# Kernel tuning notes

Measured on AMD Instinct MI355X. Metric: run time of the kernel, lower is better.

The kernel has to match this reference:

```python
import jax, jax.numpy as jnp
import numpy as np

B, T, D = 4, 8192, 1024
H = 16
HD = D // H  # 64
TOP_K = 64


def setup_inputs() -> dict:
    key = jax.random.key(0)
    ks = jax.random.split(key, 6)
    x = jax.random.normal(ks[0], (B, T, D), dtype=jnp.float32)
    # torch nn.Linear weights are [out, in]; y = x @ W.T
    Wq = jax.random.normal(ks[1], (D, D), dtype=jnp.float32) * 0.02
    Wk = jax.random.normal(ks[2], (D, D), dtype=jnp.float32) * 0.02
    Wv = jax.random.normal(ks[3], (D, D), dtype=jnp.float32) * 0.02
    Wo = jax.random.normal(ks[4], (D, D), dtype=jnp.float32) * 0.02
    # indexer: nn.Linear(head_dim, 1, bias=False) -> weight [1, HD]; keep as [HD]
    w_score = jax.random.normal(ks[5], (HD,), dtype=jnp.float32) * 0.02
    return {"x": x, "Wq": Wq, "Wk": Wk, "Wv": Wv, "Wo": Wo, "w_score": w_score}


def reference(x, Wq, Wk, Wv, Wo, w_score):
    b, t, d = x.shape
    top_k = min(TOP_K, t)
    # projections: [B,T,D] -> [B,H,T,HD]
    def proj(W):
        return jnp.einsum('btd,ed->bte', x, W).reshape(b, t, H, HD).transpose(0, 2, 1, 3)
    q = proj(Wq)
    k = proj(Wk)
    v = proj(Wv)
    # lightning indexer scores: [B,H,T]
    idx_scores = jnp.einsum('bhtd,d->bht', k, w_score)
    _, top_idx = jax.lax.top_k(idx_scores, top_k)  # [B,H,K]
    idx = top_idx[..., None]  # [B,H,K,1]
    k_sparse = jnp.take_along_axis(k, idx, axis=2)  # [B,H,K,HD]
    v_sparse = jnp.take_along_axis(v, idx, axis=2)
    scale = HD ** -0.5
    scores = jnp.einsum('bhtd,bhkd->bhtk', q, k_sparse) * scale  # [B,H,T,K]
    attn = jax.nn.softmax(scores, axis=-1)
    out = jnp.einsum('bhtk,bhkd->bhtd', attn, v_sparse)  # [B,H,T,HD]
    out = out.transpose(0, 2, 1, 3).reshape(b, t, d)
    return jnp.einsum('btd,ed->bte', out, Wo)
```

## Files before the change

### kernel.cpp

```cpp
#include <hip/hip_runtime.h>
#include <hip/hip_bf16.h>
#include <stdint.h>

#define NB 4
#define NT 8192
#define ND 1024
#define NH 16
#define NHD 64
#define NK 64
#define NM (NB*NT)

typedef __attribute__((ext_vector_type(4))) float f32x4;
typedef __attribute__((ext_vector_type(8))) short s16x8;
typedef const void __attribute__((address_space(1)))* gas1_t;
typedef void __attribute__((address_space(3)))* las3_t;

__device__ __forceinline__ float bf2f(ushort u) {
  union { uint32_t i; float f; } v; v.i = ((uint32_t)u) << 16; return v.f;
}
__device__ __forceinline__ ushort f2bf(float f) {
  union { float f; uint32_t i; } v; v.f = f;
  uint32_t r = v.i + 0x7FFFu + ((v.i >> 16) & 1u);
  return (ushort)(r >> 16);
}
__device__ __forceinline__ uint32_t f2ord(uint32_t u) {
  return (u & 0x80000000u) ? ~u : (u | 0x80000000u);
}

__global__ __launch_bounds__(256) void convert_w_kernel(
    const float* __restrict__ Wq, const float* __restrict__ Wk,
    const float* __restrict__ Wv, const float* __restrict__ Wo,
    ushort* __restrict__ wqb, ushort* __restrict__ wkb,
    ushort* __restrict__ wvb, ushort* __restrict__ wob) {
  int i = blockIdx.x * 256 + threadIdx.x;
  wqb[i] = f2bf(Wq[i]); wkb[i] = f2bf(Wk[i]);
  wvb[i] = f2bf(Wv[i]); wob[i] = f2bf(Wo[i]);
}

__global__ __launch_bounds__(256) void prep_u_kernel(
    const float* __restrict__ Wk, const float* __restrict__ wscore,
    ushort* __restrict__ uhi, ushort* __restrict__ ulo) {
  int e = (blockIdx.x & 3) * 256 + threadIdx.x;
  int h = blockIdx.x >> 2;
  float acc = 0.f;
  #pragma unroll 8
  for (int d = 0; d < NHD; ++d) acc += wscore[d] * Wk[(size_t)(h*NHD + d)*ND + e];
  ushort hv = f2bf(acc);
  uhi[h*ND + e] = hv;
  ulo[h*ND + e] = f2bf(acc - bf2f(hv));
}

__global__ __launch_bounds__(256) void prep_x_kernel(
    const float* __restrict__ x, const ushort* __restrict__ uhi,
    const ushort* __restrict__ ulo, ushort* __restrict__ xb,
    float* __restrict__ scores) {
  __shared__ __align__(16) ushort Ahi[32 * 128];
  __shared__ __align__(16) ushort Alo[32 * 128];
  __shared__ float red[4][2][16][17];
  int t = threadIdx.x, w = t >> 6, l = t & 63;
  int tok0 = blockIdx.x * 32;
  int srow = t >> 3;
  int sg = (t & 7) * 2;
  int rs = l & 15, ks8 = (l >> 4) * 8;
  f32x4 acc[2];
  acc[0] = (f32x4){0.f,0.f,0.f,0.f};
  acc[1] = (f32x4){0.f,0.f,0.f,0.f};
  for (int kc = 0; kc < 8; ++kc) {
    int kb = kc * 128;
    {
      const float* xr = x + (size_t)(tok0 + srow) * ND + kb + sg * 8;
      f32x4 v0 = *(const f32x4*)xr;
      f32x4 v1 = *(const f32x4*)(xr + 4);
      f32x4 v2 = *(const f32x4*)(xr + 8);
      f32x4 v3 = *(const f32x4*)(xr + 12);
      s16x8 hi0, lo0, hi1, lo1;
      #pragma unroll
      for (int j = 0; j < 4; ++j) {
        ushort h;
        h = f2bf(v0[j]); hi0[j]   = (short)h; lo0[j]   = (short)f2bf(v0[j] - bf2f(h));
        h = f2bf(v1[j]); hi0[4+j] = (short)h; lo0[4+j] = (short)f2bf(v1[j] - bf2f(h));
        h = f2bf(v2[j]); hi1[j]   = (short)h; lo1[j]   = (short)f2bf(v2[j] - bf2f(h));
        h = f2bf(v3[j]); hi1[4+j] = (short)h; lo1[4+j] = (short)f2bf(v3[j] - bf2f(h));
      }
      ushort* xo = xb + (size_t)(tok0 + srow) * ND + kb + sg * 8;
      *(s16x8*)xo = hi0;
      *(s16x8*)(xo + 8) = hi1;
      int p0 = (sg ^ (srow & 7)) * 8, p1 = ((sg + 1) ^ (srow & 7)) * 8;
      *(s16x8*)&Ahi[srow*128 + p0] = hi0;
      *(s16x8*)&Ahi[srow*128 + p1] = hi1;
      *(s16x8*)&Alo[srow*128 + p0] = lo0;
      *(s16x8*)&Alo[srow*128 + p1] = lo1;
    }
    __syncthreads();
    {
      s16x8 bh = *(const s16x8*)(uhi + rs * ND + kb + w * 32 + ks8);
      s16x8 bl = *(const s16x8*)(ulo + rs * ND + kb + w * 32 + ks8);
      int gl = w * 4 + (l >> 4);
      #pragma unroll
      for (int mi = 0; mi < 2; ++mi) {
        int row = mi * 16 + rs;
        int gp = (gl ^ (row & 7)) * 8;
        s16x8 ah = *(const s16x8*)&Ahi[row*128 + gp];
        s16x8 al = *(const s16x8*)&Alo[row*128 + gp];
        acc[mi] = __builtin_amdgcn_mfma_f32_16x16x32_bf16(ah, bh, acc[mi], 0, 0, 0);
        acc[mi] = __builtin_amdgcn_mfma_f32_16x16x32_bf16(al, bh, acc[mi], 0, 0, 0);
        acc[mi] = __builtin_amdgcn_mfma_f32_16x16x32_bf16(ah, bl, acc[mi], 0, 0, 0);
      }
    }
    __syncthreads();
  }
  #pragma unroll
  for (int mi = 0; mi < 2; ++mi)
    #pragma unroll
    for (int r = 0; r < 4; ++r)
      red[w][mi][(l >> 4) * 4 + r][l & 15] = acc[mi][r];
  __syncthreads();
  int boff = ((tok0 >> 13) << 4);
  int tt0 = tok0 & (NT - 1);
  #pragma unroll
  for (int it = 0; it < 2; ++it) {
    int tok = t & 31, h = (t >> 5) + it * 8;
    int mi = tok >> 4, row = tok & 15;
    float s = red[0][mi][row][h] + red[1][mi][row][h]
            + red[2][mi][row][h] + red[3][mi][row][h];
    scores[(size_t)(boff + h) * NT + tt0 + tok] = s;
  }
}

__global__ __launch_bounds__(256) void topk_kernel(
    const float* __restrict__ scores, int* __restrict__ tidx) {
  int bh = blockIdx.x, t = threadIdx.x;
  __shared__ uint32_t keys[NT];
  __shared__ int hist[4096];
  __shared__ uint32_t ck[512];
  __shared__ int ci[512];
  __shared__ int chunksum[256];
  __shared__ int s_binB, s_c0;
  __shared__ int cnt_hi, cnt_cand;

  for (int i = t; i < 4096; i += 256) hist[i] = 0;
  if (t == 0) { cnt_hi = 0; cnt_cand = 0; }
  __syncthreads();
  const uint4* sg = (const uint4*)(scores + (size_t)bh * NT);
  for (int i = t; i < NT/4; i += 256) {
    uint4 v = sg[i];
    uint32_t k0 = f2ord(v.x), k1 = f2ord(v.y), k2 = f2ord(v.z), k3 = f2ord(v.w);
    keys[i*4+0] = k0; keys[i*4+1] = k1; keys[i*4+2] = k2; keys[i*4+3] = k3;
    atomicAdd(&hist[k0 >> 20], 1); atomicAdd(&hist[k1 >> 20], 1);
    atomicAdd(&hist[k2 >> 20], 1); atomicAdd(&hist[k3 >> 20], 1);
  }
  __syncthreads();
  {
    int hi = 4095 - t * 16;
    int s = 0;
    #pragma unroll
    for (int j = 0; j < 16; ++j) s += hist[hi - j];
    chunksum[t] = s;
  }
  __syncthreads();
  if (t == 0) {
    int cum = 0, c = 0;
    while (cum + chunksum[c] < NK) { cum += chunksum[c]; ++c; }
    int bin = 4095 - c * 16;
    while (cum + hist[bin] < NK) { cum += hist[bin]; --bin; }
    s_binB = bin; s_c0 = cum;
  }
  __syncthreads();
  int binB = s_binB, c0 = s_c0;
  for (int i = t; i < NT; i += 256) {
    int b = keys[i] >> 20;
    if (b > binB) {
      int p = atomicAdd(&cnt_hi, 1);
      tidx[bh*NK + p] = i;
    } else if (b == binB) {
      int p = atomicAdd(&cnt_cand, 1);
      if (p < 512) { ck[p] = keys[i]; ci[p] = i; }
    }
  }
  __syncthreads();
  int nc = cnt_cand; if (nc > 512) nc = 512;
  int need = NK - c0;
  for (int p = t; p < nc; p += 256) {
    uint32_t myk = ck[p]; int myi = ci[p];
    int rank = 0;
    for (int j = 0; j < nc; ++j) {
      uint32_t kj = ck[j];
      rank += (kj > myk || (kj == myk && ci[j] < myi)) ? 1 : 0;
    }
    if (rank < need) tidx[bh*NK + c0 + rank] = myi;
  }
}

__global__ __launch_bounds__(256, 4) void sparse_kv_kernel(
    const ushort* __restrict__ xb, const ushort* __restrict__ wkb,
    const ushort* __restrict__ wvb, const int* __restrict__ tidx,
    ushort* __restrict__ ksp, ushort* __restrict__ vtsp) {
  int bh = blockIdx.x, gy = blockIdx.y;
  int b = bh >> 4, h = bh & 15;
  int t = threadIdx.x;
  __shared__ __align__(16) ushort xl[16][128];
  __shared__ int kid[16];
  if (t < 16) kid[t] = tidx[bh*NK + gy*16 + t];
  int d = t & 63, kq = t >> 6;
  float ak[4] = {0.f,0.f,0.f,0.f}, av[4] = {0.f,0.f,0.f,0.f};
  const ushort* wkr = wkb + (size_t)(h*NHD + d) * ND;
  const ushort* wvr = wvb + (size_t)(h*NHD + d) * ND;
  for (int kc = 0; kc < ND; kc += 128) {
    __syncthreads();
    {
      int row = t >> 4, c8 = (t & 15) * 8;
      *(uint4*)&xl[row][c8] = *(const uint4*)(xb + (size_t)(b*NT + kid[row]) * ND + kc + c8);
    }
    __syncthreads();
    #pragma unroll 1
    for (int sub = 0; sub < 8; ++sub) {
      s16x8 k0 = *(const s16x8*)(wkr + kc + sub*16);
      s16x8 k1 = *(const s16x8*)(wkr + kc + sub*16 + 8);
      s16x8 v0 = *(const s16x8*)(wvr + kc + sub*16);
      s16x8 v1 = *(const s16x8*)(wvr + kc + sub*16 + 8);
      float kf[16], vf2[16];
      #pragma unroll
      for (int j = 0; j < 8; ++j) {
        kf[j]  = bf2f((ushort)k0[j]); kf[8+j]  = bf2f((ushort)k1[j]);
        vf2[j] = bf2f((ushort)v0[j]); vf2[8+j] = bf2f((ushort)v1[j]);
      }
      #pragma unroll
      for (int kk = 0; kk < 4; ++kk) {
        #pragma unroll
        for (int j = 0; j < 16; ++j) {
          float xvv = bf2f(xl[kq*4 + kk][sub*16 + j]);
          ak[kk] += xvv * kf[j];
          av[kk] += xvv * vf2[j];
        }
      }
    }
  }
  #pragma unroll
  for (int kk = 0; kk < 4; ++kk) {
    int key = gy*16 + kq*4 + kk;
    ksp[((size_t)bh*NK + key)*NHD + d] = f2bf(ak[kk]);
    vtsp[((size_t)bh*NHD + d)*NK + key] = f2bf(av[kk]);
  }
}

template<int STORE_BF16>
__global__ __launch_bounds__(512, 2) void gemm8_kernel(
    const ushort* __restrict__ A, const ushort* __restrict__ Bw,
    void* __restrict__ Cout) {
  __shared__ __align__(16) char lds[131072];
  const int t = threadIdx.x, wid = t >> 6, l = t & 63;
  const int wr = wid >> 2, wc = wid & 3;
  int bid = blockIdx.x;
  int wg = (bid & 7) * 64 + (bid >> 3);
  int tm = wg >> 2, tn = wg & 3;
  const int K = 1024, N = 1024;
  const ushort* Ab = A + (size_t)tm * 256 * K;
  const ushort* Bb = Bw + (size_t)tn * 256 * K;
  const int skh  = ((l & 3) * 8) ^ (((l >> 5) & 1) << 4);
  const int srow = l >> 2;
  const int lane_off = (l & 15) * 64 + ((((l >> 4) * 8) ^ (((l >> 3) & 1) << 4)) * 2);
  f32x4 acc[8][4];
  #pragma unroll
  for (int i = 0; i < 8; ++i)
    #pragma unroll
    for (int j = 0; j < 4; ++j) acc[i][j] = (f32x4){0.f, 0.f, 0.f, 0.f};
  s16x8 afr[4][2], bfr[2][2];

#define STG(gbase, matoff, half, ktile, buf) do { \
    const ushort* _s = (gbase) + (size_t)((half)*128 + wid*16 + srow) * K + (ktile)*64 + skh; \
    int _d = (buf)*65536 + (matoff) + ((half)*128 + wid*16)*64; \
    __builtin_amdgcn_global_load_lds((gas1_t)_s, (las3_t)(lds + _d), 16, 0, 0); \
    __builtin_amdgcn_global_load_lds((gas1_t)(_s + 32), (las3_t)(lds + _d + 16384), 16, 0, 0); \
  } while (0)

#define RD_A(mh, kh, buf) do { \
    _Pragma("unroll") \
    for (int mi = 0; mi < 4; ++mi) \
      afr[mi][kh] = *(const s16x8*)(lds + (buf)*65536 + (kh)*16384 + \
                      ((((mh)*2 + wr)*64 + mi*16))*64 + lane_off); \
  } while (0)

#define RD_B(nh, kh, buf) do { \
    _Pragma("unroll") \
    for (int ni = 0; ni < 2; ++ni) \
      bfr[ni][kh] = *(const s16x8*)(lds + (buf)*65536 + 32768 + (kh)*16384 + \
                      (((nh)*128 + wc*32 + ni*16))*64 + lane_off); \
  } while (0)

#define MMAQH(mh, nh, kh) do { \
    __builtin_amdgcn_s_setprio(1); \
    _Pragma("unroll") \
    for (int mi = 0; mi < 4; ++mi) \
      _Pragma("unroll") \
      for (int ni = 0; ni < 2; ++ni) \
        acc[(mh)*4+mi][(nh)*2+ni] = __builtin_amdgcn_mfma_f32_16x16x32_bf16( \
            afr[mi][kh], bfr[ni][kh], acc[(mh)*4+mi][(nh)*2+ni], 0, 0, 0); \
    __builtin_amdgcn_s_setprio(0); \
  } while (0)

#define LG0() do { asm volatile("s_waitcnt lgkmcnt(0)" ::: "memory"); \
                   __builtin_amdgcn_sched_barrier(0); } while (0)
#define ENDPH() do { __builtin_amdgcn_sched_barrier(0); \
                     __builtin_amdgcn_s_barrier(); } while (0)

#define TILE(kt, bc, bn) do { \
  LG0(); MMAQH(0,0,0); RD_A(0,1,bc); RD_B(0,1,bc); ENDPH(); \
  LG0(); MMAQH(0,0,1); RD_B(1,0,bc); \
  if ((kt)+1 < 16) STG(Bb,32768,0,(kt)+1,bn); ENDPH(); \
  LG0(); MMAQH(0,1,0); RD_B(1,1,bc); ENDPH(); \
  LG0(); MMAQH(0,1,1); RD_A(1,0,bc); \
  if ((kt)+2 < 16) STG(Ab,0,0,(kt)+2,bc); ENDPH(); \
  LG0(); MMAQH(1,1,0); RD_A(1,1,bc); ENDPH(); \
  LG0(); MMAQH(1,1,1); RD_B(0,0,bc); \
  if ((kt)+2 < 16) STG(Bb,32768,1,(kt)+2,bc); ENDPH(); \
  LG0(); MMAQH(1,0,0); RD_B(0,1,bc); ENDPH(); \
  LG0(); MMAQH(1,0,1); \
  if ((kt) < 14)       { asm volatile("s_waitcnt vmcnt(4)" ::: "memory"); } \
  else if ((kt) == 14) { asm volatile("s_waitcnt vmcnt(0)" ::: "memory"); } \
  __builtin_amdgcn_sched_barrier(0); \
  __builtin_amdgcn_s_barrier(); \
  if ((kt)+1 < 16) { RD_A(0,0,bn); RD_B(0,0,bn); } \
  if ((kt)+2 < 16) STG(Ab,0,1,(kt)+2,bc); \
} while (0)

  STG(Ab,0,0,0,0); STG(Bb,32768,0,0,0); STG(Ab,0,1,0,0); STG(Bb,32768,1,0,0);
  STG(Ab,0,0,1,1); STG(Bb,32768,1,1,1); STG(Ab,0,1,1,1);
  asm volatile("s_waitcnt vmcnt(6)" ::: "memory");
  __builtin_amdgcn_s_barrier();
  RD_A(0,0,0); RD_B(0,0,0);

  for (int k2 = 0; k2 < 8; ++k2) {
    TILE(2*k2,     0, 1);
    TILE(2*k2 + 1, 1, 0);
  }
#undef TILE
#undef STG
#undef RD_A
#undef RD_B
#undef MMAQH
#undef LG0
#undef ENDPH

  #pragma unroll
  for (int mi8 = 0; mi8 < 8; ++mi8) {
    int grow = tm*256 + (((mi8 >> 2)*2 + wr)*64) + (mi8 & 3)*16 + (l >> 4)*4;
    #pragma unroll
    for (int ni4 = 0; ni4 < 4; ++ni4) {
      int gcol = tn*256 + (ni4 >> 1)*128 + wc*32 + (ni4 & 1)*16 + (l & 15);
      #pragma unroll
      for (int r = 0; r < 4; ++r) {
        size_t off = (size_t)(grow + r) * N + gcol;
        if (STORE_BF16) ((ushort*)Cout)[off] = f2bf(acc[mi8][ni4][r]);
        else            ((float*)Cout)[off]  = acc[mi8][ni4][r];
      }
    }
  }
}

__global__ __launch_bounds__(256, 2) void attn_kernel(
    const ushort* __restrict__ qg, const ushort* __restrict__ ksp,
    const ushort* __restrict__ vtsp, ushort* __restrict__ aout) {
  int bh = blockIdx.y;
  int b = bh >> 4, h = bh & 15;
  int t = threadIdx.x, w = t >> 6, l = t & 63;
  __shared__ __align__(16) ushort Pl[4][1024];
  const ushort* kb = ksp + (size_t)bh * NK * NHD;
  const ushort* vb = vtsp + (size_t)bh * NHD * NK;
  s16x8 kf[2][4], vf[2][4];
  #pragma unroll
  for (int ks = 0; ks < 2; ++ks)
    #pragma unroll
    for (int ni = 0; ni < 4; ++ni) {
      kf[ks][ni] = *(const s16x8*)&kb[(size_t)(ni*16 + (l & 15))*NHD + ks*32 + (l >> 4)*8];
      vf[ks][ni] = *(const s16x8*)&vb[(size_t)(ni*16 + (l & 15))*NK + ks*32 + (l >> 4)*8];
    }
  int rowbase = blockIdx.x * 256 + w * 64;
  #pragma unroll 1
  for (int mi = 0; mi < 4; ++mi) {
    int r0 = rowbase + mi * 16;
    s16x8 af[2];
    #pragma unroll
    for (int ks = 0; ks < 2; ++ks)
      af[ks] = *(const s16x8*)&qg[(size_t)(b*NT + r0 + (l & 15))*ND + h*NHD + ks*32 + (l >> 4)*8];
    f32x4 sc[4];
    #pragma unroll
    for (int ni = 0; ni < 4; ++ni) {
      f32x4 z; z[0]=0.f; z[1]=0.f; z[2]=0.f; z[3]=0.f;
      z = __builtin_amdgcn_mfma_f32_16x16x32_bf16(af[0], kf[0][ni], z, 0, 0, 0);
      sc[ni] = __builtin_amdgcn_mfma_f32_16x16x32_bf16(af[1], kf[1][ni], z, 0, 0, 0);
    }
    #pragma unroll
    for (int r = 0; r < 4; ++r) {
      float v0 = sc[0][r]*0.125f, v1 = sc[1][r]*0.125f;
      float v2 = sc[2][r]*0.125f, v3 = sc[3][r]*0.125f;
      float m = fmaxf(fmaxf(v0, v1), fmaxf(v2, v3));
      #pragma unroll
      for (int mm = 8; mm >= 1; mm >>= 1) m = fmaxf(m, __shfl_xor(m, mm, 64));
      float e0 = __expf(v0 - m), e1 = __expf(v1 - m);
      float e2 = __expf(v2 - m), e3 = __expf(v3 - m);
      float s = e0 + e1 + e2 + e3;
      #pragma unroll
      for (int mm = 8; mm >= 1; mm >>= 1) s += __shfl_xor(s, mm, 64);
      float inv = 1.f / s;
      int prow = (l >> 4)*4 + r;
      int lo = l & 7, hb = (l >> 3) & 1, sw = prow & 7;
      Pl[w][prow*64 + ((0 + hb) ^ sw)*8 + lo] = f2bf(e0 * inv);
      Pl[w][prow*64 + ((2 + hb) ^ sw)*8 + lo] = f2bf(e1 * inv);
      Pl[w][prow*64 + ((4 + hb) ^ sw)*8 + lo] = f2bf(e2 * inv);
      Pl[w][prow*64 + ((6 + hb) ^ sw)*8 + lo] = f2bf(e3 * inv);
    }
    s16x8 pf[2];
    #pragma unroll
    for (int ks = 0; ks < 2; ++ks)
      pf[ks] = *(const s16x8*)&Pl[w][(l & 15)*64 + ((ks*4 + (l >> 4)) ^ (l & 7))*8];
    f32x4 oc[4];
    #pragma unroll
    for (int ni = 0; ni < 4; ++ni) {
      f32x4 z; z[0]=0.f; z[1]=0.f; z[2]=0.f; z[3]=0.f;
      z = __builtin_amdgcn_mfma_f32_16x16x32_bf16(pf[0], vf[0][ni], z, 0, 0, 0);
      oc[ni] = __builtin_amdgcn_mfma_f32_16x16x32_bf16(pf[1], vf[1][ni], z, 0, 0, 0);
    }
    #pragma unroll
    for (int ni = 0; ni < 4; ++ni)
      #pragma unroll
      for (int r = 0; r < 4; ++r) {
        int row = r0 + (l >> 4)*4 + r;
        aout[(size_t)(b*NT + row)*ND + h*NHD + ni*16 + (l & 15)] = f2bf(oc[ni][r]);
      }
  }
}

extern "C" void kernel_launch(void* const* d_in, const int* in_sizes, int n_in,
                              void* d_out, int out_size, void* d_ws, size_t ws_size,
                              hipStream_t stream) {
  (void)in_sizes; (void)n_in; (void)out_size; (void)ws_size;
  const float* x  = (const float*)d_in[0];
  const float* Wq = (const float*)d_in[1];
  const float* Wk = (const float*)d_in[2];
  const float* Wv = (const float*)d_in[3];
  const float* Wo = (const float*)d_in[4];
  const float* wscore = (const float*)d_in[5];

  char* base = (char*)d_ws;
  ushort* xb     = (ushort*)(base + 0);
  ushort* qb     = (ushort*)(base + 67108864);
  float*  scores = (float*) (base + 134217728);
  ushort* uhi    = (ushort*)(base + 136314880);
  ushort* ulo    = (ushort*)(base + 136347648);
  ushort* wqb    = (ushort*)(base + 136380416);
  ushort* wkb    = (ushort*)(base + 138477568);
  ushort* wvb    = (ushort*)(base + 140574720);
  ushort* wob    = (ushort*)(base + 142671872);
  int*    tidx   = (int*)   (base + 144769024);
  ushort* ksp    = (ushort*)(base + 144785408);
  ushort* vtsp   = (ushort*)(base + 145309696);
  ushort* aout   = xb;

  convert_w_kernel<<<dim3(4096), dim3(256), 0, stream>>>(Wq, Wk, Wv, Wo, wqb, wkb, wvb, wob);
  prep_u_kernel<<<dim3(64), dim3(256), 0, stream>>>(Wk, wscore, uhi, ulo);
  prep_x_kernel<<<dim3(1024), dim3(256), 0, stream>>>(x, uhi, ulo, xb, scores);
  topk_kernel<<<dim3(64), dim3(256), 0, stream>>>(scores, tidx);
  sparse_kv_kernel<<<dim3(64, 4), dim3(256), 0, stream>>>(xb, wkb, wvb, tidx, ksp, vtsp);
  gemm8_kernel<1><<<dim3(512), dim3(512), 0, stream>>>(xb, wqb, (void*)qb);
  attn_kernel<<<dim3(32, 64), dim3(256), 0, stream>>>(qb, ksp, vtsp, aout);
  gemm8_kernel<0><<<dim3(512), dim3(512), 0, stream>>>(aout, wob, d_out);
}
```

Measured before the change: 292.7 us.

## Restructure GEMM main loop into two-phase k-half schedule with fewer barriers

```diff
diff --git a/kernel.cpp b/kernel.cpp
--- a/kernel.cpp
+++ b/kernel.cpp
@@ -264,7 +264,7 @@
   for (int i = 0; i < 8; ++i)
     #pragma unroll
     for (int j = 0; j < 4; ++j) acc[i][j] = (f32x4){0.f, 0.f, 0.f, 0.f};
-  s16x8 afr[4][2], bfr[2][2];
+  s16x8 aS[2][8], bS[2][4];
 
 #define STG(gbase, matoff, half, ktile, buf) do { \
     const ushort* _s = (gbase) + (size_t)((half)*128 + wid*16 + srow) * K + (ktile)*64 + skh; \
@@ -273,73 +273,74 @@
     __builtin_amdgcn_global_load_lds((gas1_t)(_s + 32), (las3_t)(lds + _d + 16384), 16, 0, 0); \
   } while (0)
 
-#define RD_A(mh, kh, buf) do { \
+#define STGALL(ktile, buf) do { \
+    STG(Ab, 0, 0, ktile, buf);     STG(Ab, 0, 1, ktile, buf); \
+    STG(Bb, 32768, 0, ktile, buf); STG(Bb, 32768, 1, ktile, buf); \
+  } while (0)
+
+#define RD_ALLX(kh, buf) do { \
     _Pragma("unroll") \
-    for (int mi = 0; mi < 4; ++mi) \
-      afr[mi][kh] = *(const s16x8*)(lds + (buf)*65536 + (kh)*16384 + \
-                      ((((mh)*2 + wr)*64 + mi*16))*64 + lane_off); \
+    for (int mh = 0; mh < 2; ++mh) \
+      _Pragma("unroll") \
+      for (int mi = 0; mi < 4; ++mi) \
+        aS[kh][mh*4+mi] = *(const s16x8*)(lds + (buf)*65536 + (kh)*16384 + \
+                          ((mh*2 + wr)*64 + mi*16)*64 + lane_off); \
+    _Pragma("unroll") \
+    for (int nh = 0; nh < 2; ++nh) \
+      _Pragma("unroll") \
+      for (int ni = 0; ni < 2; ++ni) \
+        bS[kh][nh*2+ni] = *(const s16x8*)(lds + (buf)*65536 + 32768 + (kh)*16384 + \
+                          ((nh*128 + wc*32 + ni*16))*64 + lane_off); \
   } while (0)
 
-#define RD_B(nh, kh, buf) do { \
-    _Pragma("unroll") \
-    for (int ni = 0; ni < 2; ++ni) \
-      bfr[ni][kh] = *(const s16x8*)(lds + (buf)*65536 + 32768 + (kh)*16384 + \
-                      (((nh)*128 + wc*32 + ni*16))*64 + lane_off); \
-  } while (0)
-
-#define MMAQH(mh, nh, kh) do { \
+#define MM32(kh) do { \
     __builtin_amdgcn_s_setprio(1); \
     _Pragma("unroll") \
-    for (int mi = 0; mi < 4; ++mi) \
+    for (int mf = 0; mf < 8; ++mf) \
       _Pragma("unroll") \
-      for (int ni = 0; ni < 2; ++ni) \
-        acc[(mh)*4+mi][(nh)*2+ni] = __builtin_amdgcn_mfma_f32_16x16x32_bf16( \
-            afr[mi][kh], bfr[ni][kh], acc[(mh)*4+mi][(nh)*2+ni], 0, 0, 0); \
+      for (int nf = 0; nf < 4; ++nf) \
+        acc[mf][nf] = __builtin_amdgcn_mfma_f32_16x16x32_bf16( \
+            aS[kh][mf], bS[kh][nf], acc[mf][nf], 0, 0, 0); \
     __builtin_amdgcn_s_setprio(0); \
   } while (0)
 
-#define LG0() do { asm volatile("s_waitcnt lgkmcnt(0)" ::: "memory"); \
-                   __builtin_amdgcn_sched_barrier(0); } while (0)
-#define ENDPH() do { __builtin_amdgcn_sched_barrier(0); \
-                     __builtin_amdgcn_s_barrier(); } while (0)
-
-#define TILE(kt, bc, bn) do { \
-  LG0(); MMAQH(0,0,0); RD_A(0,1,bc); RD_B(0,1,bc); ENDPH(); \
-  LG0(); MMAQH(0,0,1); RD_B(1,0,bc); \
-  if ((kt)+1 < 16) STG(Bb,32768,0,(kt)+1,bn); ENDPH(); \
-  LG0(); MMAQH(0,1,0); RD_B(1,1,bc); ENDPH(); \
-  LG0(); MMAQH(0,1,1); RD_A(1,0,bc); \
-  if ((kt)+2 < 16) STG(Ab,0,0,(kt)+2,bc); ENDPH(); \
-  LG0(); MMAQH(1,1,0); RD_A(1,1,bc); ENDPH(); \
-  LG0(); MMAQH(1,1,1); RD_B(0,0,bc); \
-  if ((kt)+2 < 16) STG(Bb,32768,1,(kt)+2,bc); ENDPH(); \
-  LG0(); MMAQH(1,0,0); RD_B(0,1,bc); ENDPH(); \
-  LG0(); MMAQH(1,0,1); \
-  if ((kt) < 14)       { asm volatile("s_waitcnt vmcnt(4)" ::: "memory"); } \
+#define BODY(kt, bc, bn) do { \
+  RD_ALLX(1, bc);                        \
+  MM32(0);                               \
+  asm volatile("s_waitcnt lgkmcnt(0)" ::: "memory"); \
+  __builtin_amdgcn_sched_barrier(0); \
+  __builtin_amdgcn_s_barrier();          \
+  __builtin_amdgcn_sched_barrier(0); \
+  if ((kt) + 2 < 16) STGALL((kt) + 2, bc); \
+  if ((kt) < 14)       { asm volatile("s_waitcnt vmcnt(8)" ::: "memory"); } \
   else if ((kt) == 14) { asm volatile("s_waitcnt vmcnt(0)" ::: "memory"); } \
   __builtin_amdgcn_sched_barrier(0); \
-  __builtin_amdgcn_s_barrier(); \
-  if ((kt)+1 < 16) { RD_A(0,0,bn); RD_B(0,0,bn); } \
-  if ((kt)+2 < 16) STG(Ab,0,1,(kt)+2,bc); \
+  if ((kt) < 15) { \
+    __builtin_amdgcn_s_barrier();        \
+    __builtin_amdgcn_sched_barrier(0); \
+    RD_ALLX(0, bn);                      \
+  } \
+  MM32(1);                               \
+  __builtin_amdgcn_sched_barrier(0);     \
 } while (0)
 
-  STG(Ab,0,0,0,0); STG(Bb,32768,0,0,0); STG(Ab,0,1,0,0); STG(Bb,32768,1,0,0);
-  STG(Ab,0,0,1,1); STG(Bb,32768,1,1,1); STG(Ab,0,1,1,1);
-  asm volatile("s_waitcnt vmcnt(6)" ::: "memory");
+  STGALL(0, 0);
+  STGALL(1, 1);
+  asm volatile("s_waitcnt vmcnt(8)" ::: "memory");
+  __builtin_amdgcn_sched_barrier(0);
   __builtin_amdgcn_s_barrier();
-  RD_A(0,0,0); RD_B(0,0,0);
+  __builtin_amdgcn_sched_barrier(0);
+  RD_ALLX(0, 0);
 
   for (int k2 = 0; k2 < 8; ++k2) {
-    TILE(2*k2,     0, 1);
-    TILE(2*k2 + 1, 1, 0);
-  }
-#undef TILE
+    BODY(2*k2,     0, 1);
+    BODY(2*k2 + 1, 1, 0);
+  }
+#undef BODY
+#undef MM32
+#undef RD_ALLX
+#undef STGALL
 #undef STG
-#undef RD_A
-#undef RD_B
-#undef MMAQH
-#undef LG0
-#undef ENDPH
 
   #pragma unroll
   for (int mi8 = 0; mi8 < 8; ++mi8) {
```

New measurement: 399.0 us. +36.3%, slower.

## Fuse top-k selection with MFMA sparse K/V projection, merge prep_u into convert

Applied to the files above, without the earlier changes.

```diff
diff --git a/kernel.cpp b/kernel.cpp
--- a/kernel.cpp
+++ b/kernel.cpp
@@ -30,24 +30,23 @@
 __global__ __launch_bounds__(256) void convert_w_kernel(
     const float* __restrict__ Wq, const float* __restrict__ Wk,
     const float* __restrict__ Wv, const float* __restrict__ Wo,
+    const float* __restrict__ wscore,
     ushort* __restrict__ wqb, ushort* __restrict__ wkb,
-    ushort* __restrict__ wvb, ushort* __restrict__ wob) {
+    ushort* __restrict__ wvb, ushort* __restrict__ wob,
+    ushort* __restrict__ uhi, ushort* __restrict__ ulo) {
   int i = blockIdx.x * 256 + threadIdx.x;
   wqb[i] = f2bf(Wq[i]); wkb[i] = f2bf(Wk[i]);
   wvb[i] = f2bf(Wv[i]); wob[i] = f2bf(Wo[i]);
-}
-
-__global__ __launch_bounds__(256) void prep_u_kernel(
-    const float* __restrict__ Wk, const float* __restrict__ wscore,
-    ushort* __restrict__ uhi, ushort* __restrict__ ulo) {
-  int e = (blockIdx.x & 3) * 256 + threadIdx.x;
-  int h = blockIdx.x >> 2;
-  float acc = 0.f;
-  #pragma unroll 8
-  for (int d = 0; d < NHD; ++d) acc += wscore[d] * Wk[(size_t)(h*NHD + d)*ND + e];
-  ushort hv = f2bf(acc);
-  uhi[h*ND + e] = hv;
-  ulo[h*ND + e] = f2bf(acc - bf2f(hv));
+  if (blockIdx.x < 64) {
+    int e = (blockIdx.x & 3) * 256 + threadIdx.x;
+    int h = blockIdx.x >> 2;
+    float acc = 0.f;
+    #pragma unroll 8
+    for (int d = 0; d < NHD; ++d) acc += wscore[d] * Wk[(size_t)(h*NHD + d)*ND + e];
+    ushort hv = f2bf(acc);
+    uhi[h*ND + e] = hv;
+    ulo[h*ND + e] = f2bf(acc - bf2f(hv));
+  }
 }
 
 __global__ __launch_bounds__(256) void prep_x_kernel(
@@ -127,9 +126,12 @@
   }
 }
 
-__global__ __launch_bounds__(256) void topk_kernel(
-    const float* __restrict__ scores, int* __restrict__ tidx) {
+__global__ __launch_bounds__(256) void topsel_kv_kernel(
+    const float* __restrict__ scores, const ushort* __restrict__ xb,
+    const ushort* __restrict__ wkb, const ushort* __restrict__ wvb,
+    ushort* __restrict__ ksp, ushort* __restrict__ vtsp) {
   int bh = blockIdx.x, t = threadIdx.x;
+  int b = bh >> 4, h = bh & 15;
   __shared__ uint32_t keys[NT];
   __shared__ int hist[4096];
   __shared__ uint32_t ck[512];
@@ -137,6 +139,9 @@
   __shared__ int chunksum[256];
   __shared__ int s_binB, s_c0;
   __shared__ int cnt_hi, cnt_cand;
+  __shared__ int kid[64];
+  __shared__ __align__(16) ushort Xs[64 * 128];
+  __shared__ __align__(16) ushort Ws[2][64 * 128];
 
   for (int i = t; i < 4096; i += 256) hist[i] = 0;
   if (t == 0) { cnt_hi = 0; cnt_cand = 0; }
@@ -168,11 +173,11 @@
   __syncthreads();
   int binB = s_binB, c0 = s_c0;
   for (int i = t; i < NT; i += 256) {
-    int b = keys[i] >> 20;
-    if (b > binB) {
+    int bb = keys[i] >> 20;
+    if (bb > binB) {
       int p = atomicAdd(&cnt_hi, 1);
-      tidx[bh*NK + p] = i;
-    } else if (b == binB) {
+      kid[p] = i;
+    } else if (bb == binB) {
       int p = atomicAdd(&cnt_cand, 1);
       if (p < 512) { ck[p] = keys[i]; ci[p] = i; }
     }
@@ -187,60 +192,69 @@
       uint32_t kj = ck[j];
       rank += (kj > myk || (kj == myk && ci[j] < myi)) ? 1 : 0;
     }
-    if (rank < need) tidx[bh*NK + c0 + rank] = myi;
-  }
-}
-
-__global__ __launch_bounds__(256, 4) void sparse_kv_kernel(
-    const ushort* __restrict__ xb, const ushort* __restrict__ wkb,
-    const ushort* __restrict__ wvb, const int* __restrict__ tidx,
-    ushort* __restrict__ ksp, ushort* __restrict__ vtsp) {
-  int bh = blockIdx.x, gy = blockIdx.y;
-  int b = bh >> 4, h = bh & 15;
-  int t = threadIdx.x;
-  __shared__ __align__(16) ushort xl[16][128];
-  __shared__ int kid[16];
-  if (t < 16) kid[t] = tidx[bh*NK + gy*16 + t];
-  int d = t & 63, kq = t >> 6;
-  float ak[4] = {0.f,0.f,0.f,0.f}, av[4] = {0.f,0.f,0.f,0.f};
-  const ushort* wkr = wkb + (size_t)(h*NHD + d) * ND;
-  const ushort* wvr = wvb + (size_t)(h*NHD + d) * ND;
+    if (rank < need) kid[c0 + rank] = myi;
+  }
+
+  int w = t >> 6, l = t & 63;
+  int sel = w >> 1, nb = (w & 1) * 32;
+  f32x4 acc[4][2];
+  #pragma unroll
+  for (int mi = 0; mi < 4; ++mi)
+    #pragma unroll
+    for (int ni = 0; ni < 2; ++ni) acc[mi][ni] = (f32x4){0.f,0.f,0.f,0.f};
+  int srow = t >> 2;
+  int gj = (t & 3) * 4;
   for (int kc = 0; kc < ND; kc += 128) {
     __syncthreads();
-    {
-      int row = t >> 4, c8 = (t & 15) * 8;
-      *(uint4*)&xl[row][c8] = *(const uint4*)(xb + (size_t)(b*NT + kid[row]) * ND + kc + c8);
+    const ushort* xr  = xb  + (size_t)(b*NT + kid[srow]) * ND + kc;
+    const ushort* wkr = wkb + (size_t)(h*NHD + srow) * ND + kc;
+    const ushort* wvr = wvb + (size_t)(h*NHD + srow) * ND + kc;
+    #pragma unroll
+    for (int j = 0; j < 4; ++j) {
+      int p = ((gj + j) ^ (srow & 7)) * 8;
+      *(uint4*)&Xs[srow*128 + p]    = *(const uint4*)(xr  + (gj + j) * 8);
+      *(uint4*)&Ws[0][srow*128 + p] = *(const uint4*)(wkr + (gj + j) * 8);
+      *(uint4*)&Ws[1][srow*128 + p] = *(const uint4*)(wvr + (gj + j) * 8);
     }
     __syncthreads();
-    #pragma unroll 1
-    for (int sub = 0; sub < 8; ++sub) {
-      s16x8 k0 = *(const s16x8*)(wkr + kc + sub*16);
-      s16x8 k1 = *(const s16x8*)(wkr + kc + sub*16 + 8);
-      s16x8 v0 = *(const s16x8*)(wvr + kc + sub*16);
-      s16x8 v1 = *(const s16x8*)(wvr + kc + sub*16 + 8);
-      float kf[16], vf2[16];
-      #pragma unroll
-      for (int j = 0; j < 8; ++j) {
-        kf[j]  = bf2f((ushort)k0[j]); kf[8+j]  = bf2f((ushort)k1[j]);
-        vf2[j] = bf2f((ushort)v0[j]); vf2[8+j] = bf2f((ushort)v1[j]);
-      }
-      #pragma unroll
-      for (int kk = 0; kk < 4; ++kk) {
+    #pragma unroll
+    for (int ks = 0; ks < 4; ++ks) {
+      s16x8 bfr[2], afr[4];
+      #pragma unroll
+      for (int ni = 0; ni < 2; ++ni) {
+        int row = nb + ni*16 + (l & 15);
+        bfr[ni] = *(const s16x8*)&Ws[sel][row*128 + ((ks*4 + (l >> 4)) ^ (row & 7))*8];
+      }
+      #pragma unroll
+      for (int mi = 0; mi < 4; ++mi) {
+        int row = mi*16 + (l & 15);
+        afr[mi] = *(const s16x8*)&Xs[row*128 + ((ks*4 + (l >> 4)) ^ (row & 7))*8];
+      }
+      #pragma unroll
+      for (int mi = 0; mi < 4; ++mi)
         #pragma unroll
-        for (int j = 0; j < 16; ++j) {
-          float xvv = bf2f(xl[kq*4 + kk][sub*16 + j]);
-          ak[kk] += xvv * kf[j];
-          av[kk] += xvv * vf2[j];
-        }
-      }
-    }
-  }
-  #pragma unroll
-  for (int kk = 0; kk < 4; ++kk) {
-    int key = gy*16 + kq*4 + kk;
-    ksp[((size_t)bh*NK + key)*NHD + d] = f2bf(ak[kk]);
-    vtsp[((size_t)bh*NHD + d)*NK + key] = f2bf(av[kk]);
-  }
+        for (int ni = 0; ni < 2; ++ni)
+          acc[mi][ni] = __builtin_amdgcn_mfma_f32_16x16x32_bf16(
+              afr[mi], bfr[ni], acc[mi][ni], 0, 0, 0);
+    }
+  }
+  #pragma unroll
+  for (int mi = 0; mi < 4; ++mi)
+    #pragma unroll
+    for (int ni = 0; ni < 2; ++ni) {
+      int d = nb + ni*16 + (l & 15);
+      int key0 = mi*16 + (l >> 4)*4;
+      if (sel == 0) {
+        #pragma unroll
+        for (int r = 0; r < 4; ++r)
+          ksp[((size_t)bh*NK + key0 + r)*NHD + d] = f2bf(acc[mi][ni][r]);
+      } else {
+        ushort4 o;
+        o.x = f2bf(acc[mi][ni][0]); o.y = f2bf(acc[mi][ni][1]);
+        o.z = f2bf(acc[mi][ni][2]); o.w = f2bf(acc[mi][ni][3]);
+        *(ushort4*)&vtsp[((size_t)bh*NHD + d)*NK + key0] = o;
+      }
+    }
 }
 
 template<int STORE_BF16>
@@ -451,16 +465,14 @@
   ushort* wkb    = (ushort*)(base + 138477568);
   ushort* wvb    = (ushort*)(base + 140574720);
   ushort* wob    = (ushort*)(base + 142671872);
-  int*    tidx   = (int*)   (base + 144769024);
   ushort* ksp    = (ushort*)(base + 144785408);
   ushort* vtsp   = (ushort*)(base + 145309696);
   ushort* aout   = xb;
 
-  convert_w_kernel<<<dim3(4096), dim3(256), 0, stream>>>(Wq, Wk, Wv, Wo, wqb, wkb, wvb, wob);
-  prep_u_kernel<<<dim3(64), dim3(256), 0, stream>>>(Wk, wscore, uhi, ulo);
+  convert_w_kernel<<<dim3(4096), dim3(256), 0, stream>>>(
+      Wq, Wk, Wv, Wo, wscore, wqb, wkb, wvb, wob, uhi, ulo);
   prep_x_kernel<<<dim3(1024), dim3(256), 0, stream>>>(x, uhi, ulo, xb, scores);
-  topk_kernel<<<dim3(64), dim3(256), 0, stream>>>(scores, tidx);
-  sparse_kv_kernel<<<dim3(64, 4), dim3(256), 0, stream>>>(xb, wkb, wvb, tidx, ksp, vtsp);
+  topsel_kv_kernel<<<dim3(64), dim3(256), 0, stream>>>(scores, xb, wkb, wvb, ksp, vtsp);
   gemm8_kernel<1><<<dim3(512), dim3(512), 0, stream>>>(xb, wqb, (void*)qb);
   attn_kernel<<<dim3(32, 64), dim3(256), 0, stream>>>(qb, ksp, vtsp, aout);
   gemm8_kernel<0><<<dim3(512), dim3(512), 0, stream>>>(aout, wob, d_out);
```

Result: faster. 263.2 us (median of 2 runs) (-10.1%).
